# Optimization experiments

Hardware: AMD Instinct MI355X
Metric: run time of the kernel (lower is better)

Reference implementation:

```python
import jax, jax.numpy as jnp
import numpy as np

D = 1024
H = 16
DK = D // H

def setup_inputs() -> dict:
    key = jax.random.key(0)
    k1, k2, k3 = jax.random.split(key, 3)
    x = jax.random.normal(k1, (2, 2048, D), dtype=jnp.float32)
    # torch nn.Linear weight shapes: qkv [3D, D], o [D, D]; y = x @ W.T
    scale = 1.0 / np.sqrt(D)
    W_qkv = jax.random.normal(k2, (3 * D, D), dtype=jnp.float32) * scale
    W_o = jax.random.normal(k3, (D, D), dtype=jnp.float32) * scale
    return {"x": x, "W_qkv": W_qkv, "W_o": W_o}

def reference(x, W_qkv, W_o):
    B, T, _ = x.shape
    qkv = x @ W_qkv.T                                    # [B, T, 3D]
    qkv = qkv.reshape(B, T, 3, H, DK)
    qkv = jnp.transpose(qkv, (0, 3, 2, 1, 4))            # [B, H, 3, T, DK]
    q, k, v = qkv[:, :, 0], qkv[:, :, 1], qkv[:, :, 2]   # each [B, H, T, DK]
    scores = jnp.einsum("bhqd,bhkd->bhqk", q, k) / np.sqrt(DK)
    causal = jnp.tril(jnp.ones((T, T), dtype=bool))       # keep lower triangle
    scores = jnp.where(causal, scores, -jnp.inf)
    attn = jax.nn.softmax(scores, axis=-1)
    out = jnp.einsum("bhqk,bhkd->bhqd", attn, v)          # [B, H, T, DK]
    out = jnp.transpose(out, (0, 2, 1, 3)).reshape(B, T, H * DK)
    return out @ W_o.T
```

## Files before the change

### kernel.cpp

```cpp
#include <hip/hip_runtime.h>
#include <hip/hip_bf16.h>

typedef __bf16 bf16x8 __attribute__((ext_vector_type(8)));
typedef float f32x4 __attribute__((ext_vector_type(4)));
typedef unsigned int u32;
typedef u32 u32x4 __attribute__((ext_vector_type(4)));

#define MFMA(a, b, c) __builtin_amdgcn_mfma_f32_16x16x32_bf16((a), (b), (c), 0, 0, 0)

static __device__ __forceinline__ bf16x8 ld8(const __bf16* p) {
  return *reinterpret_cast<const bf16x8*>(p);
}

static __device__ __forceinline__ u32 pkbf(float a, float b) {
  union { __bf16 h; unsigned short s; } x, y;
  x.h = (__bf16)a; y.h = (__bf16)b;
  return (u32)x.s | ((u32)y.s << 16);
}

typedef unsigned int __attribute__((address_space(1))) gu32_t;
typedef unsigned int __attribute__((address_space(3))) lu32_t;
static __device__ __forceinline__ void gld16(const __bf16* g, __bf16* l) {
  __builtin_amdgcn_global_load_lds((const gu32_t*)(const void*)g,
                                   (lu32_t*)(void*)l, 16, 0, 0);
}

__global__ __launch_bounds__(256)
void cvt_f32_bf16(const float* __restrict__ a, __bf16* __restrict__ oa, int na,
                  const float* __restrict__ b, __bf16* __restrict__ ob) {
  const int i = blockIdx.x * 256 + threadIdx.x;
  const float* src; __bf16* dst; int e;
  if (i < (na >> 3)) { src = a; dst = oa; e = i << 3; }
  else { src = b; dst = ob; e = (i << 3) - na; }
  f32x4 v0 = *reinterpret_cast<const f32x4*>(src + e);
  f32x4 v1 = *reinterpret_cast<const f32x4*>(src + e + 4);
  bf16x8 o;
#pragma unroll
  for (int j = 0; j < 4; ++j) { o[j] = (__bf16)v0[j]; o[j + 4] = (__bf16)v1[j]; }
  *reinterpret_cast<bf16x8*>(dst + e) = o;
}

static __device__ __forceinline__ void stage8f(__bf16* __restrict__ dst,
                                               const float* __restrict__ src) {
  f32x4 a = *reinterpret_cast<const f32x4*>(src);
  f32x4 b = *reinterpret_cast<const f32x4*>(src + 4);
  bf16x8 o;
#pragma unroll
  for (int i = 0; i < 4; ++i) { o[i] = (__bf16)a[i]; o[i + 4] = (__bf16)b[i]; }
  *reinterpret_cast<bf16x8*>(dst) = o;
}

template<int BN, bool SPLIT, bool OUT_BF16, bool B_F32>
__global__ __launch_bounds__(256, 2)
void gemm3(const __bf16* __restrict__ A, const void* __restrict__ Wv,
           void* __restrict__ Cv, __bf16* __restrict__ VT,
           int M, int N, int K) {
  constexpr int NF = BN / 32;
  constexpr float SC2Q = 0.125f * 1.4426950408889634f;
  __shared__ __bf16 lA[128 * 64];
  __shared__ __bf16 lB[BN * 64];

  const int tid = threadIdx.x;
  const int ntiles = N / BN;
  const int mt = blockIdx.x / ntiles;
  const int nt = blockIdx.x % ntiles;
  const int m0 = mt << 7, n0 = nt * BN;
  const int lane = tid & 63, w = tid >> 6;
  const int wm = (w >> 1) << 6;
  const int wn = (w & 1) * (BN / 2);
  const int fr = lane & 15, fg = lane >> 4;

  f32x4 acc[4][NF] = {};

  for (int k0 = 0; k0 < K; k0 += 64) {
    __syncthreads();
#pragma unroll
    for (int jj = 0; jj < 4; ++jj) {
      const int q = (w << 2) | jj;
      const int v = (q << 6) | lane;
      const int row = v >> 3;
      const int cc = (v & 7) ^ (row & 7);
      gld16(A + (size_t)(m0 + row) * K + k0 + (cc << 3), lA + (q << 9));
    }
    if constexpr (B_F32) {
#pragma unroll
      for (int hh = 0; hh < BN / 64; ++hh) {
        const int row = (tid >> 2) + (hh << 6);
        const int c0 = (tid & 3) << 1;
        const float* src = (const float*)Wv + (size_t)(n0 + row) * K + k0 + (c0 << 3);
#pragma unroll
        for (int cg = 0; cg < 2; ++cg)
          stage8f(lB + (row << 6) + (((c0 + cg) ^ (row & 7)) << 3), src + (cg << 3));
      }
    } else {
#pragma unroll
      for (int jj = 0; jj < NF; ++jj) {
        const int q = w * NF + jj;
        const int v = (q << 6) | lane;
        const int row = v >> 3;
        const int cc = (v & 7) ^ (row & 7);
        gld16((const __bf16*)Wv + (size_t)(n0 + row) * K + k0 + (cc << 3), lB + (q << 9));
      }
    }
    __syncthreads();

    bf16x8 af[2][4], bfr[2][NF];
#pragma unroll
    for (int kc = 0; kc < 2; ++kc) {
#pragma unroll
      for (int m = 0; m < 4; ++m) {
        const int row = wm + m * 16 + fr;
        af[kc][m] = ld8(lA + (row << 6) + ((((kc << 2) | fg) ^ (row & 7)) << 3));
      }
#pragma unroll
      for (int n = 0; n < NF; ++n) {
        const int row = wn + n * 16 + fr;
        bfr[kc][n] = ld8(lB + (row << 6) + ((((kc << 2) | fg) ^ (row & 7)) << 3));
      }
    }
#pragma unroll
    for (int kc = 0; kc < 2; ++kc)
#pragma unroll
      for (int m = 0; m < 4; ++m)
#pragma unroll
        for (int n = 0; n < NF; ++n)
          acc[m][n] = MFMA(af[kc][m], bfr[kc][n], acc[m][n]);
  }

#pragma unroll
  for (int m = 0; m < 4; ++m) {
#pragma unroll
    for (int n = 0; n < NF; ++n) {
#pragma unroll
      for (int r = 0; r < 4; ++r) {
        int row = m0 + wm + m * 16 + fg * 4 + r;
        int col = n0 + wn + n * 16 + fr;
        float v = acc[m][n][r];
        if constexpr (SPLIT) {
          int b = row >> 11, t = row & 2047;
          if (col >= 2048) {
            VT[((size_t)(b << 10) + (col - 2048)) * 2048 + t] = (__bf16)v;
          } else {
            if (col < 1024) v *= SC2Q;
            ((__bf16*)Cv)[(size_t)row * 2048 + col] = (__bf16)v;
          }
        } else if constexpr (OUT_BF16) {
          ((__bf16*)Cv)[(size_t)row * N + col] = (__bf16)v;
        } else {
          ((float*)Cv)[(size_t)row * N + col] = v;
        }
      }
    }
  }
}

static __device__ __forceinline__ void softmax_step(
    f32x4 (&s)[4], f32x4 (&o)[4], float& m, float& l, bf16x8 (&pa)[2],
    bool diag, int q0wt, int k0, int fg, int fr) {
  constexpr float NEG = -1e30f;
  float sv[4][4];
#pragma unroll
  for (int n = 0; n < 4; ++n)
#pragma unroll
    for (int r = 0; r < 4; ++r) {
      float x = s[n][r];
      if (diag && (k0 + n * 16 + fg * 4 + r > q0wt + fr)) x = NEG;
      sv[n][r] = x;
    }

  float t0 = fmaxf(fmaxf(sv[0][0], sv[0][1]), fmaxf(sv[0][2], sv[0][3]));
  float t1 = fmaxf(fmaxf(sv[1][0], sv[1][1]), fmaxf(sv[1][2], sv[1][3]));
  float t2 = fmaxf(fmaxf(sv[2][0], sv[2][1]), fmaxf(sv[2][2], sv[2][3]));
  float t3 = fmaxf(fmaxf(sv[3][0], sv[3][1]), fmaxf(sv[3][2], sv[3][3]));
  float rm = fmaxf(fmaxf(t0, t1), fmaxf(t2, t3));
  rm = fmaxf(rm, __shfl_xor(rm, 16));
  rm = fmaxf(rm, __shfl_xor(rm, 32));

  if (!__all(rm <= m + 16.f)) {
    float mnew = fmaxf(m, rm);
    float alpha = __builtin_exp2f(m - mnew);
    m = mnew;
    l *= alpha;
    float ao[4];
#pragma unroll
    for (int r = 0; r < 4; ++r)
      ao[r] = __shfl(alpha, fg * 4 + r);
#pragma unroll
    for (int n = 0; n < 4; ++n)
#pragma unroll
      for (int r = 0; r < 4; ++r)
        o[n][r] *= ao[r];
  }

  float p[4][4];
#pragma unroll
  for (int n = 0; n < 4; ++n)
#pragma unroll
    for (int r = 0; r < 4; ++r)
      p[n][r] = __builtin_exp2f(sv[n][r] - m);

  float u0 = (p[0][0] + p[0][1]) + (p[0][2] + p[0][3]);
  float u1 = (p[1][0] + p[1][1]) + (p[1][2] + p[1][3]);
  float u2 = (p[2][0] + p[2][1]) + (p[2][2] + p[2][3]);
  float u3 = (p[3][0] + p[3][1]) + (p[3][2] + p[3][3]);
  float rs = (u0 + u1) + (u2 + u3);
  rs += __shfl_xor(rs, 16);
  rs += __shfl_xor(rs, 32);
  l += rs;

  u32 wpk[4][2];
#pragma unroll
  for (int n = 0; n < 4; ++n) {
    wpk[n][0] = pkbf(p[n][0], p[n][1]);
    wpk[n][1] = pkbf(p[n][2], p[n][3]);
  }

  u32 rcv[2][2][2];
#pragma unroll
  for (int e = 0; e < 2; ++e) {
    const int src = fr + ((((fg & 1) << 1) | ((fg >> 1) ^ e)) << 4);
    const bool tsel = ((fg & 1) ^ e) != 0;
#pragma unroll
    for (int c = 0; c < 2; ++c)
#pragma unroll
      for (int hh = 0; hh < 2; ++hh) {
        u32 v = tsel ? wpk[(c << 1) | 1][hh] : wpk[(c << 1) | 0][hh];
        rcv[e][c][hh] = (u32)__shfl((int)v, src);
      }
  }
  const bool hi = (fg >> 1) != 0;
  u32x4 w0, w1;
#pragma unroll
  for (int a = 0; a < 2; ++a)
#pragma unroll
    for (int hh = 0; hh < 2; ++hh) {
      w0[2 * a + hh] = hi ? rcv[a ^ 1][0][hh] : rcv[a][0][hh];
      w1[2 * a + hh] = hi ? rcv[a ^ 1][1][hh] : rcv[a][1][hh];
    }
  pa[0] = __builtin_bit_cast(bf16x8, w0);
  pa[1] = __builtin_bit_cast(bf16x8, w1);
}

static __device__ __forceinline__ void write_out(
    __bf16* __restrict__ out, f32x4 (&o)[4], float l,
    int b, int hoff, int q0wt, int fg, int fr) {
  float linv = 1.f / l;
  float lo[4];
#pragma unroll
  for (int r = 0; r < 4; ++r)
    lo[r] = __shfl(linv, fg * 4 + r);
#pragma unroll
  for (int n = 0; n < 4; ++n)
#pragma unroll
    for (int r = 0; r < 4; ++r) {
      int t = q0wt + fg * 4 + r;
      out[((size_t)(b * 2048 + t)) * 1024 + hoff + n * 16 + fr] = (__bf16)(o[n][r] * lo[r]);
    }
}

__global__ __launch_bounds__(256, 2)
void attn_causal7(const __bf16* __restrict__ qk, const __bf16* __restrict__ vt,
                  __bf16* __restrict__ out) {
  constexpr float NEG = -1e30f;

  __shared__ __bf16 lK[2][4096];
  __shared__ __bf16 lV[2][4096];

  const int tid = threadIdx.x;
  const int lane = tid & 63, w = tid >> 6;
  const int fr = lane & 15, fg = lane >> 4;
  const int blk = blockIdx.x;
  const int rest = blk >> 3;
  const int bh = ((blk & 7) << 2) | (rest & 3);
  const int i = rest >> 2;
  const int qb0 = 31 - i, qb1 = i;
  const int b = bh >> 4, h = bh & 15;
  const int q0w0 = (qb0 << 6) + (w << 4);
  const int q0w1 = (qb1 << 6) + (w << 4);
  const int hoff = h * 64;
  const size_t qkbase = (size_t)b * (2048 * 2048);
  const __bf16* kb = qk + qkbase + 1024 + hoff;
  const __bf16* vtb = vt + (size_t)((b << 10) | hoff) * 2048;

  bf16x8 qf0[2], qf1[2];
#pragma unroll
  for (int c = 0; c < 2; ++c) {
    qf0[c] = ld8(qk + qkbase + (size_t)(q0w0 + fr) * 2048 + hoff + c * 32 + fg * 8);
    qf1[c] = ld8(qk + qkbase + (size_t)(q0w1 + fr) * 2048 + hoff + c * 32 + fg * 8);
  }

  f32x4 o0[4] = {}, o1[4] = {};
  float m_0 = NEG, l_0 = 0.f, m_1 = NEG, l_1 = 0.f;

#define STAGE(bf, k0s)                                                        \
  do {                                                                        \
    _Pragma("unroll")                                                         \
    for (int jj = 0; jj < 2; ++jj) {                                          \
      const int q = (w << 1) | jj;                                            \
      const int v = (q << 6) | lane;                                          \
      const int row = v >> 3;                                                 \
      const int cc = (v & 7) ^ (row & 7);                                     \
      gld16(kb + (size_t)((k0s) + row) * 2048 + (cc << 3), &lK[bf][q << 9]);  \
      gld16(vtb + (size_t)row * 2048 + (k0s) + (cc << 3), &lV[bf][q << 9]);   \
    }                                                                         \
  } while (0)

  int buf = 0;
  STAGE(0, 0);
  __syncthreads();

  for (int kt = 0; kt <= qb0; ++kt) {
    const int k0 = kt << 6;
    if (kt < qb0) STAGE(buf ^ 1, k0 + 64);
    const bool act1 = (kt <= qb1);

    f32x4 s0[4] = {}, s1[4] = {};
#pragma unroll
    for (int c = 0; c < 2; ++c) {
      bf16x8 kfc[4];
#pragma unroll
      for (int n = 0; n < 4; ++n) {
        const int row = n * 16 + fr;
        const int sc = ((c << 2) | fg) ^ (row & 7);
        kfc[n] = ld8(&lK[buf][(row << 6) + (sc << 3)]);
      }
#pragma unroll
      for (int n = 0; n < 4; ++n)
        s0[n] = MFMA(kfc[n], qf0[c], s0[n]);
      if (act1) {
#pragma unroll
        for (int n = 0; n < 4; ++n)
          s1[n] = MFMA(kfc[n], qf1[c], s1[n]);
      }
    }

    bf16x8 pa0[2], pa1[2];
    softmax_step(s0, o0, m_0, l_0, pa0, kt == qb0, q0w0, k0, fg, fr);
    if (act1)
      softmax_step(s1, o1, m_1, l_1, pa1, kt == qb1, q0w1, k0, fg, fr);

#pragma unroll
    for (int c = 0; c < 2; ++c) {
      bf16x8 vfc[4];
#pragma unroll
      for (int n = 0; n < 4; ++n) {
        const int row = n * 16 + fr;
        const int sc = ((c << 2) | fg) ^ (row & 7);
        vfc[n] = ld8(&lV[buf][(row << 6) + (sc << 3)]);
      }
#pragma unroll
      for (int n = 0; n < 4; ++n)
        o0[n] = MFMA(pa0[c], vfc[n], o0[n]);
      if (act1) {
#pragma unroll
        for (int n = 0; n < 4; ++n)
          o1[n] = MFMA(pa1[c], vfc[n], o1[n]);
      }
    }

    __syncthreads();
    buf ^= 1;
  }
#undef STAGE

  write_out(out, o0, l_0, b, hoff, q0w0, fg, fr);
  write_out(out, o1, l_1, b, hoff, q0w1, fg, fr);
}

extern "C" void kernel_launch(void* const* d_in, const int* in_sizes, int n_in,
                              void* d_out, int out_size, void* d_ws, size_t ws_size,
                              hipStream_t stream) {
  const float* x = (const float*)d_in[0];
  const float* w_qkv = (const float*)d_in[1];
  const float* w_o = (const float*)d_in[2];
  float* out = (float*)d_out;

  const int M = 4096;
  __bf16* qk = (__bf16*)d_ws;
  __bf16* vt = (__bf16*)((char*)d_ws + (size_t)M * 2048 * 2);
  __bf16* attn = (__bf16*)((char*)d_ws + (size_t)M * 3072 * 2);

  __bf16* xb = (__bf16*)d_out;
  __bf16* wqb = xb + 4194304;
  const int NX = 4194304;

  cvt_f32_bf16<<<3584, 256, 0, stream>>>(x, xb, NX, w_qkv, wqb);

  gemm3<128, true, true, false><<<(M / 128) * (3072 / 128), 256, 0, stream>>>(
      xb, (const void*)wqb, (void*)qk, vt, M, 3072, 1024);

  attn_causal7<<<512, 256, 0, stream>>>(qk, vt, attn);

  gemm3<64, false, false, true><<<(M / 128) * (1024 / 64), 256, 0, stream>>>(
      attn, (const void*)w_o, (void*)out, nullptr, M, 1024, 1024);
}
```

Measured before the change: 127.1 us.

## Split causal attention KV loop across two blocks and combine partials

The attention kernel is split so that each (head, query-pair) work item is handled by two blocks. Each block processes alternating KV tiles and writes normalized partial outputs plus log-sum-exp values to scratch buffers, reusing d_out and workspace memory. A new combine kernel merges the two partials into the final attention output. This doubles the grid from 512 to 1024 blocks and raises the occupancy hint to fill the GPU better. In exchange it adds an extra launch and extra global traffic for the partials, and the bf16 partials can lose some precision.

```diff
diff --git a/kernel.cpp b/kernel.cpp
--- a/kernel.cpp
+++ b/kernel.cpp
@@ -241,10 +241,12 @@
   pa[1] = __builtin_bit_cast(bf16x8, w1);
 }
 
-static __device__ __forceinline__ void write_out(
-    __bf16* __restrict__ out, f32x4 (&o)[4], float l,
-    int b, int hoff, int q0wt, int fg, int fr) {
-  float linv = 1.f / l;
+static __device__ __forceinline__ void write_partial(
+    __bf16* __restrict__ pbase, float* __restrict__ sbase,
+    f32x4 (&o)[4], float m, float l, int w, int fg, int fr) {
+  const float linv = (l > 0.f) ? 1.f / l : 0.f;
+  const float s = (l > 0.f) ? m + __builtin_log2f(l) : -1e30f;
+  if (fg == 0) sbase[w * 16 + fr] = s;
   float lo[4];
 #pragma unroll
   for (int r = 0; r < 4; ++r)
@@ -252,15 +254,13 @@
 #pragma unroll
   for (int n = 0; n < 4; ++n)
 #pragma unroll
-    for (int r = 0; r < 4; ++r) {
-      int t = q0wt + fg * 4 + r;
-      out[((size_t)(b * 2048 + t)) * 1024 + hoff + n * 16 + fr] = (__bf16)(o[n][r] * lo[r]);
-    }
-}
-
-__global__ __launch_bounds__(256, 2)
-void attn_causal7(const __bf16* __restrict__ qk, const __bf16* __restrict__ vt,
-                  __bf16* __restrict__ out) {
+    for (int r = 0; r < 4; ++r)
+      pbase[(w * 16 + fg * 4 + r) * 64 + n * 16 + fr] = (__bf16)(o[n][r] * lo[r]);
+}
+
+__global__ __launch_bounds__(256, 4)
+void attn_split8(const __bf16* __restrict__ qk, const __bf16* __restrict__ vt,
+                 __bf16* __restrict__ pbuf, float* __restrict__ sbuf) {
   constexpr float NEG = -1e30f;
 
   __shared__ __bf16 lK[2][4096];
@@ -270,10 +270,12 @@
   const int lane = tid & 63, w = tid >> 6;
   const int fr = lane & 15, fg = lane >> 4;
   const int blk = blockIdx.x;
-  const int rest = blk >> 3;
-  const int bh = ((blk & 7) << 2) | (rest & 3);
-  const int i = rest >> 2;
+  const int bh = ((blk & 7) << 2) | ((blk >> 3) & 3);
+  const int rr = blk >> 5;
+  const int i = rr & 15;
+  const int p = rr >> 4;
   const int qb0 = 31 - i, qb1 = i;
+  const int slot = bh * 16 + i;
   const int b = bh >> 4, h = bh & 15;
   const int q0w0 = (qb0 << 6) + (w << 4);
   const int q0w1 = (qb1 << 6) + (w << 4);
@@ -306,12 +308,12 @@
   } while (0)
 
   int buf = 0;
-  STAGE(0, 0);
+  STAGE(0, p << 6);
   __syncthreads();
 
-  for (int kt = 0; kt <= qb0; ++kt) {
+  for (int kt = p; kt <= qb0; kt += 2) {
     const int k0 = kt << 6;
-    if (kt < qb0) STAGE(buf ^ 1, k0 + 64);
+    if (kt + 2 <= qb0) STAGE(buf ^ 1, k0 + 128);
     const bool act1 = (kt <= qb1);
 
     f32x4 s0[4] = {}, s1[4] = {};
@@ -363,8 +365,43 @@
   }
 #undef STAGE
 
-  write_out(out, o0, l_0, b, hoff, q0w0, fg, fr);
-  write_out(out, o1, l_1, b, hoff, q0w1, fg, fr);
+  write_partial(pbuf + ((size_t)((p * 512 + slot) * 2 + 0)) * 4096,
+                sbuf + (p * 512 + slot) * 128 + 0, o0, m_0, l_0, w, fg, fr);
+  write_partial(pbuf + ((size_t)((p * 512 + slot) * 2 + 1)) * 4096,
+                sbuf + (p * 512 + slot) * 128 + 64, o1, m_1, l_1, w, fg, fr);
+}
+
+__global__ __launch_bounds__(256)
+void attn_combine(const __bf16* __restrict__ pbuf, const float* __restrict__ sbuf,
+                  __bf16* __restrict__ attn) {
+  const int u = blockIdx.x * 256 + threadIdx.x;
+  const int slot = u >> 7;
+  const int tr = u & 127;
+  const int bh = slot >> 4, i = slot & 15;
+  const int tau = tr >> 6, row = tr & 63;
+  const int qb = tau ? i : 31 - i;
+  const int t = (qb << 6) + row;
+  const int b = bh >> 4, h = bh & 15;
+
+  const float s0 = sbuf[slot * 128 + tr];
+  const float s1 = sbuf[65536 + slot * 128 + tr];
+  const float sm = fmaxf(s0, s1);
+  float w0 = __builtin_exp2f(s0 - sm), w1 = __builtin_exp2f(s1 - sm);
+  const float inv = 1.f / (w0 + w1);
+  w0 *= inv; w1 *= inv;
+
+  const __bf16* p0 = pbuf + ((size_t)(slot * 2 + tau)) * 4096 + row * 64;
+  const __bf16* p1 = p0 + (size_t)512 * 2 * 4096;
+  __bf16* dst = attn + ((size_t)(b * 2048 + t)) * 1024 + h * 64;
+#pragma unroll
+  for (int j = 0; j < 8; ++j) {
+    bf16x8 a = ld8(p0 + j * 8), c = ld8(p1 + j * 8);
+    bf16x8 o;
+#pragma unroll
+    for (int e = 0; e < 8; ++e)
+      o[e] = (__bf16)(w0 * (float)a[e] + w1 * (float)c[e]);
+    *reinterpret_cast<bf16x8*>(dst + j * 8) = o;
+  }
 }
 
 extern "C" void kernel_launch(void* const* d_in, const int* in_sizes, int n_in,
@@ -379,9 +416,11 @@
   __bf16* qk = (__bf16*)d_ws;
   __bf16* vt = (__bf16*)((char*)d_ws + (size_t)M * 2048 * 2);
   __bf16* attn = (__bf16*)((char*)d_ws + (size_t)M * 3072 * 2);
+  float* sbuf = (float*)((char*)d_ws + (size_t)33554432);
 
   __bf16* xb = (__bf16*)d_out;
   __bf16* wqb = xb + 4194304;
+  __bf16* pbuf = (__bf16*)d_out;
   const int NX = 4194304;
 
   cvt_f32_bf16<<<3584, 256, 0, stream>>>(x, xb, NX, w_qkv, wqb);
@@ -389,7 +428,9 @@
   gemm3<128, true, true, false><<<(M / 128) * (3072 / 128), 256, 0, stream>>>(
       xb, (const void*)wqb, (void*)qk, vt, M, 3072, 1024);
 
-  attn_causal7<<<512, 256, 0, stream>>>(qk, vt, attn);
+  attn_split8<<<1024, 256, 0, stream>>>(qk, vt, pbuf, sbuf);
+
+  attn_combine<<<256, 256, 0, stream>>>(pbuf, sbuf, attn);
 
   gemm3<64, false, false, true><<<(M / 128) * (1024 / 64), 256, 0, stream>>>(
       attn, (const void*)w_o, (void*)out, nullptr, M, 1024, 1024);
```

Measured after the change: 143.5 us. +12.9%, slower.

## Split paired causal q-blocks into one q-block per workgroup with higher occupancy

Applied to the files above, without the earlier changes.

Each attention workgroup previously handled two query blocks, a long one and a short one, sharing each K/V tile between them to balance causal work. Now each workgroup handles a single query block, the grid doubles to 1024 workgroups, and launch bounds ask for 4 workgroups per CU. Blocks are ordered so the longest causal rows are dispatched first. This aims for more parallelism and latency hiding, but gives up reuse of staged K/V tiles across the two query blocks, so LDS staging traffic roughly doubles.

```diff
diff --git a/kernel.cpp b/kernel.cpp
--- a/kernel.cpp
+++ b/kernel.cpp
@@ -258,9 +258,9 @@
     }
 }
 
-__global__ __launch_bounds__(256, 2)
-void attn_causal7(const __bf16* __restrict__ qk, const __bf16* __restrict__ vt,
-                  __bf16* __restrict__ out) {
+__global__ __launch_bounds__(256, 4)
+void attn_causal10(const __bf16* __restrict__ qk, const __bf16* __restrict__ vt,
+                   __bf16* __restrict__ out) {
   constexpr float NEG = -1e30f;
 
   __shared__ __bf16 lK[2][4096];
@@ -270,27 +270,24 @@
   const int lane = tid & 63, w = tid >> 6;
   const int fr = lane & 15, fg = lane >> 4;
   const int blk = blockIdx.x;
-  const int rest = blk >> 3;
-  const int bh = ((blk & 7) << 2) | (rest & 3);
-  const int i = rest >> 2;
-  const int qb0 = 31 - i, qb1 = i;
+  const int j = blk >> 3;
+  const int bh = ((blk & 7) << 2) | (j & 3);
+  const int qb = 31 - (j >> 2);
   const int b = bh >> 4, h = bh & 15;
-  const int q0w0 = (qb0 << 6) + (w << 4);
-  const int q0w1 = (qb1 << 6) + (w << 4);
+  const int q0w = (qb << 6) + (w << 4);
   const int hoff = h * 64;
   const size_t qkbase = (size_t)b * (2048 * 2048);
   const __bf16* kb = qk + qkbase + 1024 + hoff;
   const __bf16* vtb = vt + (size_t)((b << 10) | hoff) * 2048;
 
-  bf16x8 qf0[2], qf1[2];
-#pragma unroll
-  for (int c = 0; c < 2; ++c) {
-    qf0[c] = ld8(qk + qkbase + (size_t)(q0w0 + fr) * 2048 + hoff + c * 32 + fg * 8);
-    qf1[c] = ld8(qk + qkbase + (size_t)(q0w1 + fr) * 2048 + hoff + c * 32 + fg * 8);
-  }
-
-  f32x4 o0[4] = {}, o1[4] = {};
-  float m_0 = NEG, l_0 = 0.f, m_1 = NEG, l_1 = 0.f;
+  bf16x8 qf[2];
+#pragma unroll
+  for (int c = 0; c < 2; ++c)
+    qf[c] = ld8(qk + qkbase + (size_t)(q0w + fr) * 2048 + hoff + c * 32 + fg * 8);
+
+  f32x4 o[4] = {};
+  float m = NEG;
+  float l = 0.f;
 
 #define STAGE(bf, k0s)                                                        \
   do {                                                                        \
@@ -309,12 +306,11 @@
   STAGE(0, 0);
   __syncthreads();
 
-  for (int kt = 0; kt <= qb0; ++kt) {
+  for (int kt = 0; kt <= qb; ++kt) {
     const int k0 = kt << 6;
-    if (kt < qb0) STAGE(buf ^ 1, k0 + 64);
-    const bool act1 = (kt <= qb1);
-
-    f32x4 s0[4] = {}, s1[4] = {};
+    if (kt < qb) STAGE(buf ^ 1, k0 + 64);
+
+    f32x4 s[4] = {};
 #pragma unroll
     for (int c = 0; c < 2; ++c) {
       bf16x8 kfc[4];
@@ -326,18 +322,11 @@
       }
 #pragma unroll
       for (int n = 0; n < 4; ++n)
-        s0[n] = MFMA(kfc[n], qf0[c], s0[n]);
-      if (act1) {
-#pragma unroll
-        for (int n = 0; n < 4; ++n)
-          s1[n] = MFMA(kfc[n], qf1[c], s1[n]);
-      }
-    }
-
-    bf16x8 pa0[2], pa1[2];
-    softmax_step(s0, o0, m_0, l_0, pa0, kt == qb0, q0w0, k0, fg, fr);
-    if (act1)
-      softmax_step(s1, o1, m_1, l_1, pa1, kt == qb1, q0w1, k0, fg, fr);
+        s[n] = MFMA(kfc[n], qf[c], s[n]);
+    }
+
+    bf16x8 pa[2];
+    softmax_step(s, o, m, l, pa, kt == qb, q0w, k0, fg, fr);
 
 #pragma unroll
     for (int c = 0; c < 2; ++c) {
@@ -350,12 +339,7 @@
       }
 #pragma unroll
       for (int n = 0; n < 4; ++n)
-        o0[n] = MFMA(pa0[c], vfc[n], o0[n]);
-      if (act1) {
-#pragma unroll
-        for (int n = 0; n < 4; ++n)
-          o1[n] = MFMA(pa1[c], vfc[n], o1[n]);
-      }
+        o[n] = MFMA(pa[c], vfc[n], o[n]);
     }
 
     __syncthreads();
@@ -363,8 +347,7 @@
   }
 #undef STAGE
 
-  write_out(out, o0, l_0, b, hoff, q0w0, fg, fr);
-  write_out(out, o1, l_1, b, hoff, q0w1, fg, fr);
+  write_out(out, o, l, b, hoff, q0w, fg, fr);
 }
 
 extern "C" void kernel_launch(void* const* d_in, const int* in_sizes, int n_in,
@@ -389,7 +372,7 @@
   gemm3<128, true, true, false><<<(M / 128) * (3072 / 128), 256, 0, stream>>>(
       xb, (const void*)wqb, (void*)qk, vt, M, 3072, 1024);
 
-  attn_causal7<<<512, 256, 0, stream>>>(qk, vt, attn);
+  attn_causal10<<<1024, 256, 0, stream>>>(qk, vt, attn);
 
   gemm3<64, false, false, true><<<(M / 128) * (1024 / 64), 256, 0, stream>>>(
       attn, (const void*)w_o, (void*)out, nullptr, M, 1024, 1024);
```

After: 121.5 us. 4.4% less time.
